# Optimization experiments

Measured on AMD Instinct MI355X. Metric: run time of the kernel, lower is better.

## Reference

```python
import jax, jax.numpy as jnp
import numpy as np

C_DIM = 128
HIDDEN = 128
RESO = 128
PADDING = 0.1


def _resnet_block(x, w0, b0, w1, b1, ws):
    # ResnetBlockFC: net = fc_0(relu(x)); dx = fc_1(relu(net)); out = shortcut(x) + dx
    net = jnp.maximum(x, 0.0) @ w0 + b0
    dx = jnp.maximum(net, 0.0) @ w1 + b1
    return x @ ws + dx


def _scatter_mean(c, index, num_seg):
    # c: (B, T, C) float, index: (B, T) int -> (B, num_seg, C), empty bins stay 0
    def one(cb, ib):
        s = jax.ops.segment_sum(cb, ib, num_segments=num_seg)
        cnt = jax.ops.segment_sum(jnp.ones((cb.shape[0],), cb.dtype), ib, num_segments=num_seg)
        return s / jnp.maximum(cnt, 1.0)[:, None]
    return jax.vmap(one)(c, index)


def setup_inputs() -> dict:
    key = jax.random.key(0)
    ks = jax.random.split(key, 12)
    B, T, D = 2, 65536, 3
    h = HIDDEN
    p = jax.random.uniform(ks[0], (B, T, D), jnp.float32, minval=-0.5, maxval=0.5)
    s = 0.02
    fc_pos_w = jax.random.normal(ks[1], (D, 2 * h), jnp.float32) * s
    fc_pos_b = jax.random.normal(ks[2], (2 * h,), jnp.float32) * s
    # 5 ResnetBlockFC blocks, all (2h -> h) since c_dim == hidden_dim
    w0 = jax.random.normal(ks[3], (5, 2 * h, h), jnp.float32) * s
    b0 = jax.random.normal(ks[4], (5, h), jnp.float32) * s
    w1 = jax.random.normal(ks[5], (5, h, h), jnp.float32) * s
    b1 = jax.random.normal(ks[6], (5, h), jnp.float32) * s
    ws = jax.random.normal(ks[7], (5, 2 * h, h), jnp.float32) * s  # shortcut, no bias
    return {"p": p, "fc_pos_w": fc_pos_w, "fc_pos_b": fc_pos_b,
            "w0": w0, "b0": b0, "w1": w1, "b1": b1, "ws": ws}


def reference(p, fc_pos_w, fc_pos_b, w0, b0, w1, b1, ws):
    # PointNet ResNet encoder
    net = p @ fc_pos_w + fc_pos_b  # (B, T, 2h)
    for i in range(5):
        hfeat = _resnet_block(net, w0[i], b0[i], w1[i], b1[i], ws[i])  # (B, T, h)
        if i < 4:
            pooled = jnp.max(hfeat, axis=1, keepdims=True)
            net = jnp.concatenate([hfeat, jnp.broadcast_to(pooled, hfeat.shape)], axis=-1)
    c = hfeat  # (B, T, c_dim)

    # normalize_coordinate(plane='xz'): take dims (0, 2), map to [0, 1)
    xy = p[..., jnp.array([0, 2])]
    xy = xy / (1.0 + PADDING + 1e-3) + 0.5
    xy = jnp.clip(xy, 0.0, 1.0 - 1e-6)
    # coordinate2index
    xi = (xy * RESO).astype(jnp.int32)
    index = xi[..., 0] + RESO * xi[..., 1]  # (B, T)

    fea = _scatter_mean(c, index, RESO * RESO)  # (B, R*R, c_dim)
    fea_plane = jnp.transpose(fea, (0, 2, 1)).reshape(p.shape[0], C_DIM, RESO, RESO)
    return fea_plane
```

## Files before the change

### kernel.cpp

```cpp
#include <hip/hip_runtime.h>
#include <hip/hip_bf16.h>


#define G_ALL 131072
#define HD    128
#define NBINS 16384

typedef __attribute__((ext_vector_type(8))) short short8;
typedef __attribute__((ext_vector_type(4))) float f32x4;

#define MFMA16(a, b, c) __builtin_amdgcn_mfma_f32_16x16x32_bf16(a, b, c, 0, 0, 0)

__device__ __forceinline__ float bf16_to_f32(unsigned short u) {
  union { unsigned int u; float f; } v; v.u = ((unsigned int)u) << 16; return v.f;
}
__device__ __forceinline__ unsigned short f32_to_bf16(float f) {
  union { float f; unsigned int u; } v; v.f = f;
  unsigned int u = v.u;
  u += 0x7fffu + ((u >> 16) & 1u);
  return (unsigned short)(u >> 16);
}
__device__ __forceinline__ unsigned int f32_key(float f) {
  union { float f; unsigned int u; } v; v.f = f;
  return (v.u & 0x80000000u) ? ~v.u : (v.u | 0x80000000u);
}
__device__ __forceinline__ float key_f32(unsigned int k) {
  union { unsigned int u; float f; } v;
  v.u = (k & 0x80000000u) ? (k & 0x7fffffffu) : ~k;
  return v.f;
}
__device__ __forceinline__ int bin_of(float p0, float p2) {
  float x = p0 / 1.101f + 0.5f;
  x = fminf(fmaxf(x, 0.0f), 1.0f - 1e-6f);
  int xi = (int)(x * 128.0f);
  float z = p2 / 1.101f + 0.5f;
  z = fminf(fmaxf(z, 0.0f), 1.0f - 1e-6f);
  int zi = (int)(z * 128.0f);
  return xi + 128 * zi;
}
__device__ __forceinline__ short8 relu8(short8 a) {
  short8 r;
#pragma unroll
  for (int e = 0; e < 8; e++) r[e] = a[e] < 0 ? (short)0 : a[e];
  return r;
}

__global__ __launch_bounds__(128) void prep_kernel(
    const float* __restrict__ fcw, const float* __restrict__ fcb,
    const float* __restrict__ ws0, float* __restrict__ Sp,
    float* __restrict__ bsp, unsigned int* __restrict__ pool,
    int* __restrict__ hist) {
  int t = blockIdx.x * 128 + threadIdx.x;
  hist[t * 2] = 0;
  hist[t * 2 + 1] = 0;
  if (t < 1024) pool[t] = 0u;
  if (blockIdx.x == 0) {
    int j = threadIdx.x;
    for (int d = 0; d < 3; d++) {
      float s = 0.f;
      for (int ch = 0; ch < 256; ch++)
        s = fmaf(fcw[d * 256 + ch], ws0[ch * HD + j], s);
      Sp[d * HD + j] = s;
    }
    float s = 0.f;
    for (int ch = 0; ch < 256; ch++)
      s = fmaf(fcb[ch], ws0[ch * HD + j], s);
    bsp[j] = s;
  }
}

__global__ __launch_bounds__(256) void wi_kernel(
    const float* __restrict__ w0, const float* __restrict__ w1,
    const float* __restrict__ ws, const float* __restrict__ p,
    unsigned short* __restrict__ B0t, unsigned short* __restrict__ W0t,
    unsigned short* __restrict__ W1t, unsigned short* __restrict__ WSt,
    int* __restrict__ hist) {
  int gid = blockIdx.x * 256 + threadIdx.x;
  if (gid >= 245760) {
    int g = gid - 245760;
    int b = g >> 16;
    int idx = bin_of(p[3 * (size_t)g], p[3 * (size_t)g + 2]);
    atomicAdd(&hist[b * NBINS + idx], 1);
    return;
  }
  float v;
  unsigned short* dstp;
  int dst;
  if (gid < 32768) {
    int n = gid >> 8, k = gid & 255;
    v = w0[k * 128 + n];
    dstp = B0t; dst = gid;
  } else if (gid < 98304) {
    int i = gid - 32768; int s = i >> 14; int n = (i >> 7) & 127; int k = i & 127;
    v = w0[(size_t)((s + 1) * 256 + k) * 128 + n];
    dstp = W0t; dst = i;
  } else if (gid < 180224) {
    int i = gid - 98304; int s = i >> 14; int n = (i >> 7) & 127; int k = i & 127;
    v = w1[(size_t)(s * 128 + k) * 128 + n];
    dstp = W1t; dst = i;
  } else {
    int i = gid - 180224; int s = i >> 14; int n = (i >> 7) & 127; int k = i & 127;
    v = ws[(size_t)((s + 1) * 256 + k) * 128 + n];
    dstp = WSt; dst = i;
  }
  dstp[dst] = f32_to_bf16(v);
}

__global__ __launch_bounds__(1024) void scan_kernel(int* __restrict__ hist,
                                                    int* __restrict__ offsets) {
  __shared__ int sd[1024];
  int t = threadIdx.x;
  int vals[32];
  int s = 0;
#pragma unroll
  for (int i = 0; i < 32; i++) { vals[i] = hist[t * 32 + i]; s += vals[i]; }
  sd[t] = s;
  __syncthreads();
  for (int d = 1; d < 1024; d <<= 1) {
    int v = (t >= d) ? sd[t - d] : 0;
    __syncthreads();
    sd[t] += v;
    __syncthreads();
  }
  int run = sd[t] - s;
#pragma unroll
  for (int i = 0; i < 32; i++) {
    offsets[t * 32 + i] = run;
    hist[t * 32 + i] = run;
    run += vals[i];
  }
  if (t == 1023) offsets[32768] = run;
}

__global__ __launch_bounds__(256) void fill_kernel(const float* __restrict__ p,
                                                   int* __restrict__ cursor,
                                                   int* __restrict__ rank) {
  int g = blockIdx.x * 256 + threadIdx.x;
  int b = g >> 16;
  int idx = bin_of(p[3 * (size_t)g], p[3 * (size_t)g + 2]);
  int pos = atomicAdd(&cursor[b * NBINS + idx], 1);
  rank[g] = pos;
}

__global__ __launch_bounds__(256) void gather_kernel(
    const unsigned short* __restrict__ cS, const int* __restrict__ offsets,
    float* __restrict__ out) {
  __shared__ float acc[129 * 65];
  const int tid = threadIdx.x;
  const int wave = tid >> 6, lane = tid & 63;
  const int B0 = blockIdx.x * 64;
  const int b = B0 >> 14;

  for (int bi = 0; bi < 16; bi++) {
    const int binL = wave * 16 + bi;
    const int B = B0 + binL;
    const int st = offsets[B], en = offsets[B + 1];
    float a0 = 0.f, a1 = 0.f;
    int k = st;
    for (; k + 2 <= en; k += 2) {
      unsigned int u0 = *(const unsigned int*)(cS + (size_t)k * HD + lane * 2);
      unsigned int u1 = *(const unsigned int*)(cS + (size_t)(k + 1) * HD + lane * 2);
      a0 += bf16_to_f32((unsigned short)(u0 & 0xffffu));
      a1 += bf16_to_f32((unsigned short)(u0 >> 16));
      a0 += bf16_to_f32((unsigned short)(u1 & 0xffffu));
      a1 += bf16_to_f32((unsigned short)(u1 >> 16));
    }
    if (k < en) {
      unsigned int u = *(const unsigned int*)(cS + (size_t)k * HD + lane * 2);
      a0 += bf16_to_f32((unsigned short)(u & 0xffffu));
      a1 += bf16_to_f32((unsigned short)(u >> 16));
    }
    acc[(2 * lane) * 65 + binL] = a0;
    acc[(2 * lane + 1) * 65 + binL] = a1;
    if (lane == 0) acc[128 * 65 + binL] = (float)(en - st);
  }
  __syncthreads();

  const size_t outBase = (size_t)b * HD * NBINS + (size_t)(B0 & (NBINS - 1));
  const float cnt = fmaxf(acc[128 * 65 + lane], 1.0f);
#pragma unroll
  for (int c2 = 0; c2 < 32; c2++) {
    int ch = wave * 32 + c2;
    out[outBase + (size_t)ch * NBINS + lane] = acc[ch * 65 + lane] / cnt;
  }
}

__global__ __launch_bounds__(512, 4) void stage0_kernel(
    const float* __restrict__ p, const float* __restrict__ fcw,
    const float* __restrict__ fcb,
    const unsigned short* __restrict__ B0t,
    const unsigned short* __restrict__ W1t,
    const float* __restrict__ b0, const float* __restrict__ b1,
    const float* __restrict__ Sp, const float* __restrict__ bsp,
    unsigned short* __restrict__ hout, unsigned int* __restrict__ pool) {
  __shared__ float fcL[1024];
  __shared__ float ptL[64 * 5];
  __shared__ unsigned short x0t[64 * 264];
  __shared__ unsigned short m2[64 * 136];
  const int tid = threadIdx.x;
  const int lane = tid & 63;
  const int q = lane >> 4, l15 = lane & 15;
  const int nt = tid >> 6;
  const int b = blockIdx.x >> 8;
  const int wrow = nt * 16 + l15;

  short8 b0w[8], w1w[4];
#pragma unroll
  for (int kc = 0; kc < 8; kc++)
    b0w[kc] = *(const short8*)(B0t + (size_t)wrow * 256 + kc * 32 + q * 8);
#pragma unroll
  for (int kc = 0; kc < 4; kc++)
    w1w[kc] = *(const short8*)(W1t + (size_t)wrow * 128 + kc * 32 + q * 8);
  const float bias1 = b0[wrow];
  const float bias2 = bsp[wrow] + b1[wrow];
  const float sp0 = Sp[wrow], sp1 = Sp[128 + wrow], sp2 = Sp[256 + wrow];

  for (int k = tid; k < 1024; k += 512)
    fcL[k] = (k < 768) ? fcw[k] : fcb[k - 768];

  for (int it = 0; it < 4; it++) {
    const int rowBase = (blockIdx.x * 4 + it) * 64;
    __syncthreads();
    if (tid < 192) ptL[(tid / 3) * 5 + (tid % 3)] = p[(size_t)rowBase * 3 + tid];
    {
      int row = tid >> 3, c8 = tid & 7;
      const float* pr = p + (size_t)(rowBase + row) * 3;
      float p0 = pr[0], p1 = pr[1], p2 = pr[2];
#pragma unroll
      for (int cc = 0; cc < 32; cc++) {
        int ch = c8 + cc * 8;
        float x = fcL[768 + ch] + p0 * fcL[ch] + p1 * fcL[256 + ch] + p2 * fcL[512 + ch];
        x0t[row * 264 + ch] = f32_to_bf16(fmaxf(x, 0.f));
      }
    }
    __syncthreads();
    f32x4 C1[4];
#pragma unroll
    for (int s = 0; s < 4; s++) C1[s] = (f32x4){bias1, bias1, bias1, bias1};
#pragma unroll
    for (int kc = 0; kc < 8; kc++) {
#pragma unroll
      for (int s = 0; s < 4; s++) {
        short8 Ar = *(const short8*)(&x0t[(s * 16 + l15) * 264 + kc * 32 + q * 8]);
        C1[s] = MFMA16(Ar, b0w[kc], C1[s]);
      }
    }
#pragma unroll
    for (int s = 0; s < 4; s++)
#pragma unroll
      for (int r = 0; r < 4; r++)
        m2[(s * 16 + q * 4 + r) * 136 + nt * 16 + l15] =
            f32_to_bf16(fmaxf(C1[s][r], 0.f));
    __syncthreads();
    f32x4 C2[4];
#pragma unroll
    for (int s = 0; s < 4; s++)
#pragma unroll
      for (int r = 0; r < 4; r++) {
        int row = s * 16 + q * 4 + r;
        C2[s][r] = bias2 + ptL[row * 5] * sp0 + ptL[row * 5 + 1] * sp1 +
                   ptL[row * 5 + 2] * sp2;
      }
#pragma unroll
    for (int kc = 0; kc < 4; kc++) {
#pragma unroll
      for (int s = 0; s < 4; s++) {
        short8 Am = *(const short8*)(&m2[(s * 16 + l15) * 136 + kc * 32 + q * 8]);
        C2[s] = MFMA16(Am, w1w[kc], C2[s]);
      }
    }
#pragma unroll
    for (int s = 0; s < 4; s++)
#pragma unroll
      for (int r = 0; r < 4; r++)
        x0t[(s * 16 + q * 4 + r) * 136 + nt * 16 + l15] = f32_to_bf16(C2[s][r]);
    {
      float m = -1e30f;
#pragma unroll
      for (int s = 0; s < 4; s++)
#pragma unroll
        for (int r = 0; r < 4; r++) m = fmaxf(m, C2[s][r]);
      m = fmaxf(m, __shfl_xor(m, 16, 64));
      m = fmaxf(m, __shfl_xor(m, 32, 64));
      if (lane < 16) atomicMax(&pool[b * 128 + nt * 16 + lane], f32_key(m));
    }
    __syncthreads();
    {
      int r = tid >> 3, cs = (tid & 7) * 16;
      short8 v0 = *(const short8*)(&x0t[r * 136 + cs]);
      short8 v1 = *(const short8*)(&x0t[r * 136 + cs + 8]);
      *(short8*)(hout + (size_t)(rowBase + r) * 128 + cs) = v0;
      *(short8*)(hout + (size_t)(rowBase + r) * 128 + cs + 8) = v1;
    }
  }
}

__global__ __launch_bounds__(512, 4) void stageN_kernel(
    const unsigned short* __restrict__ hin, unsigned short* __restrict__ hout,
    const unsigned short* __restrict__ W0t,
    const unsigned short* __restrict__ W1t,
    const unsigned short* __restrict__ WSt,
    const float* __restrict__ b0e, const float* __restrict__ bse,
    unsigned int* __restrict__ pool, int doPool,
    const int* __restrict__ rank, int useRank) {
  __shared__ unsigned short At[64 * 136];
  __shared__ unsigned short m2[64 * 136];
  const int tid = threadIdx.x;
  const int lane = tid & 63;
  const int q = lane >> 4, l15 = lane & 15;
  const int nt = tid >> 6;
  const int b = blockIdx.x >> 8;
  const int wrow = nt * 16 + l15;

  short8 w0w[4], w1w[4], wsw[4];
#pragma unroll
  for (int kc = 0; kc < 4; kc++) {
    w0w[kc] = *(const short8*)(W0t + (size_t)wrow * 128 + kc * 32 + q * 8);
    w1w[kc] = *(const short8*)(W1t + (size_t)wrow * 128 + kc * 32 + q * 8);
    wsw[kc] = *(const short8*)(WSt + (size_t)wrow * 128 + kc * 32 + q * 8);
  }
  const float bias1 = b0e[b * 128 + wrow];
  const float bias2 = bse[b * 128 + wrow];
  const int r8 = tid >> 3, cs8 = (tid & 7) * 16;

  for (int it = 0; it < 4; it++) {
    const int rowBase = (blockIdx.x * 4 + it) * 64;
    __syncthreads();
    {
      const size_t gb = ((size_t)rowBase + r8) * 128 + cs8;
      short8 v0 = *(const short8*)(hin + gb);
      short8 v1 = *(const short8*)(hin + gb + 8);
      *(short8*)(&At[r8 * 136 + cs8]) = v0;
      *(short8*)(&At[r8 * 136 + cs8 + 8]) = v1;
    }
    __syncthreads();
    f32x4 C1[4], C2[4];
#pragma unroll
    for (int s = 0; s < 4; s++) {
      C1[s] = (f32x4){bias1, bias1, bias1, bias1};
      C2[s] = (f32x4){bias2, bias2, bias2, bias2};
    }
#pragma unroll
    for (int kc = 0; kc < 4; kc++) {
#pragma unroll
      for (int s = 0; s < 4; s++) {
        short8 Ah = *(const short8*)(&At[(s * 16 + l15) * 136 + kc * 32 + q * 8]);
        short8 Ar = relu8(Ah);
        C1[s] = MFMA16(Ar, w0w[kc], C1[s]);
        C2[s] = MFMA16(Ah, wsw[kc], C2[s]);
      }
    }
#pragma unroll
    for (int s = 0; s < 4; s++)
#pragma unroll
      for (int r = 0; r < 4; r++)
        m2[(s * 16 + q * 4 + r) * 136 + nt * 16 + l15] =
            f32_to_bf16(fmaxf(C1[s][r], 0.f));
    __syncthreads();
#pragma unroll
    for (int kc = 0; kc < 4; kc++) {
#pragma unroll
      for (int s = 0; s < 4; s++) {
        short8 Am = *(const short8*)(&m2[(s * 16 + l15) * 136 + kc * 32 + q * 8]);
        C2[s] = MFMA16(Am, w1w[kc], C2[s]);
      }
    }
    if (doPool) {
      float m = -1e30f;
#pragma unroll
      for (int s = 0; s < 4; s++)
#pragma unroll
        for (int r = 0; r < 4; r++) m = fmaxf(m, C2[s][r]);
      m = fmaxf(m, __shfl_xor(m, 16, 64));
      m = fmaxf(m, __shfl_xor(m, 32, 64));
      if (lane < 16) atomicMax(&pool[b * 128 + nt * 16 + lane], f32_key(m));
    }
#pragma unroll
    for (int s = 0; s < 4; s++)
#pragma unroll
      for (int r = 0; r < 4; r++)
        At[(s * 16 + q * 4 + r) * 136 + nt * 16 + l15] = f32_to_bf16(C2[s][r]);
    __syncthreads();
    {
      int destRow = rowBase + r8;
      if (useRank) destRow = rank[destRow];
      short8 v0 = *(const short8*)(&At[r8 * 136 + cs8]);
      short8 v1 = *(const short8*)(&At[r8 * 136 + cs8 + 8]);
      *(short8*)(hout + (size_t)destRow * 128 + cs8) = v0;
      *(short8*)(hout + (size_t)destRow * 128 + cs8 + 8) = v1;
    }
  }
}

__global__ void fold_kernel(const unsigned int* __restrict__ pool,
                            const float* __restrict__ b0s,
                            const float* __restrict__ b1s,
                            const float* __restrict__ w0hi,
                            const float* __restrict__ wshi,
                            float* __restrict__ b0e, float* __restrict__ bse) {
  __shared__ float ps[256];
  int tid = threadIdx.x;
  int b = tid >> 7, j = tid & 127;
  ps[tid] = key_f32(pool[tid]);
  __syncthreads();
  float a0 = b0s[j], a1 = b1s[j];
  for (int ch = 0; ch < 128; ch++) {
    float pv = ps[b * 128 + ch];
    a0 = fmaf(fmaxf(pv, 0.f), w0hi[ch * HD + j], a0);
    a1 = fmaf(pv, wshi[ch * HD + j], a1);
  }
  b0e[b * 128 + j] = a0;
  bse[b * 128 + j] = a1;
}

extern "C" void kernel_launch(void* const* d_in, const int* in_sizes, int n_in,
                              void* d_out, int out_size, void* d_ws,
                              size_t ws_size, hipStream_t stream) {
  const float* p   = (const float*)d_in[0];
  const float* fcw = (const float*)d_in[1];
  const float* fcb = (const float*)d_in[2];
  const float* w0  = (const float*)d_in[3];
  const float* b0  = (const float*)d_in[4];
  const float* w1  = (const float*)d_in[5];
  const float* b1  = (const float*)d_in[6];
  const float* wsc = (const float*)d_in[7];
  float* out = (float*)d_out;

  char* wsp = (char*)d_ws;
  unsigned short* hA = (unsigned short*)wsp;
  unsigned short* hB = hA + (size_t)G_ALL * HD;
  unsigned short* B0t = hB + (size_t)G_ALL * HD;
  unsigned short* W0t = B0t + 32768;
  unsigned short* W1t = W0t + 65536;
  unsigned short* WSt = W1t + 81920;
  unsigned int* pool = (unsigned int*)(WSt + 65536);
  float* b0e = (float*)(pool + 1024);
  float* bse = b0e + 1024;
  float* Sp  = bse + 1024;
  float* bsp = Sp + 384;
  int* hist    = (int*)(bsp + 128);
  int* offsets = hist + 2 * NBINS;
  int* rank    = offsets + 2 * NBINS + 4;

  prep_kernel<<<128, 128, 0, stream>>>(fcw, fcb, wsc, Sp, bsp, pool, hist);
  wi_kernel<<<1472, 256, 0, stream>>>(w0, w1, wsc, p, B0t, W0t, W1t, WSt, hist);
  scan_kernel<<<1, 1024, 0, stream>>>(hist, offsets);
  fill_kernel<<<512, 256, 0, stream>>>(p, hist, rank);

  stage0_kernel<<<512, 512, 0, stream>>>(p, fcw, fcb, B0t, W1t,
                                         b0, b1, Sp, bsp, hA, pool);
  unsigned short* hin = hA;
  unsigned short* hout = hB;
  for (int s = 1; s < 5; s++) {
    fold_kernel<<<1, 256, 0, stream>>>(
        pool + (s - 1) * 256, b0 + s * HD, b1 + s * HD,
        w0 + (size_t)(s * 256 + 128) * HD, wsc + (size_t)(s * 256 + 128) * HD,
        b0e + (s - 1) * 256, bse + (s - 1) * 256);
    stageN_kernel<<<512, 512, 0, stream>>>(
        hin, hout, W0t + (s - 1) * 16384, W1t + s * 16384,
        WSt + (s - 1) * 16384, b0e + (s - 1) * 256, bse + (s - 1) * 256,
        pool + s * 256, (s < 4) ? 1 : 0, rank, (s == 4) ? 1 : 0);
    unsigned short* t = hin; hin = hout; hout = t;
  }
  gather_kernel<<<512, 256, 0, stream>>>(hin, offsets, out);
}
```

Measured before the change: 357.6 us.

## Prefetch next tile's inputs into registers and re-pad LDS rows to 140

Both MLP stage kernels now load the next 64-row tile's inputs (points in stage0, bf16 activations in stageN) into registers while the current tile is being computed, hiding global-load latency behind the MFMA work. The LDS row stride changes from 136 to 140 shorts, altering the bank mapping of the MFMA operand reads and the transposed writes. The stage0 fc_pos expansion is also restructured to write four channels at a time with vector LDS stores. The cost is more live registers under a 512x4 launch bound, and the 140 stride breaks 16-byte alignment of short8 LDS accesses on odd rows.

New measurement: 360.0 us. No clear change (+0.7%).

```diff
diff --git a/kernel.cpp b/kernel.cpp
--- a/kernel.cpp
+++ b/kernel.cpp
@@ -7,6 +7,7 @@
 #define NBINS 16384
 
 typedef __attribute__((ext_vector_type(8))) short short8;
+typedef __attribute__((ext_vector_type(4))) short short4v;
 typedef __attribute__((ext_vector_type(4))) float f32x4;
 
 #define MFMA16(a, b, c) __builtin_amdgcn_mfma_f32_16x16x32_bf16(a, b, c, 0, 0, 0)
@@ -196,13 +197,14 @@
   __shared__ float fcL[1024];
   __shared__ float ptL[64 * 5];
   __shared__ unsigned short x0t[64 * 264];
-  __shared__ unsigned short m2[64 * 136];
+  __shared__ unsigned short m2[64 * 140];
   const int tid = threadIdx.x;
   const int lane = tid & 63;
   const int q = lane >> 4, l15 = lane & 15;
   const int nt = tid >> 6;
   const int b = blockIdx.x >> 8;
   const int wrow = nt * 16 + l15;
+  const int row8 = tid >> 3, c4 = (tid & 7) * 4;
 
   short8 b0w[8], w1w[4];
 #pragma unroll
@@ -218,20 +220,36 @@
   for (int k = tid; k < 1024; k += 512)
     fcL[k] = (k < 768) ? fcw[k] : fcb[k - 768];
 
+  float pn0, pn1, pn2, pl = 0.f;
+  {
+    const int rb = blockIdx.x * 256;
+    const float* pr = p + (size_t)(rb + row8) * 3;
+    pn0 = pr[0]; pn1 = pr[1]; pn2 = pr[2];
+    if (tid < 192) pl = p[(size_t)rb * 3 + tid];
+  }
+
   for (int it = 0; it < 4; it++) {
-    const int rowBase = (blockIdx.x * 4 + it) * 64;
-    __syncthreads();
-    if (tid < 192) ptL[(tid / 3) * 5 + (tid % 3)] = p[(size_t)rowBase * 3 + tid];
-    {
-      int row = tid >> 3, c8 = tid & 7;
-      const float* pr = p + (size_t)(rowBase + row) * 3;
-      float p0 = pr[0], p1 = pr[1], p2 = pr[2];
-#pragma unroll
-      for (int cc = 0; cc < 32; cc++) {
-        int ch = c8 + cc * 8;
-        float x = fcL[768 + ch] + p0 * fcL[ch] + p1 * fcL[256 + ch] + p2 * fcL[512 + ch];
-        x0t[row * 264 + ch] = f32_to_bf16(fmaxf(x, 0.f));
-      }
+    const int rowBase = blockIdx.x * 256 + it * 64;
+    __syncthreads();
+    if (tid < 192) ptL[(tid / 3) * 5 + (tid % 3)] = pl;
+#pragma unroll
+    for (int cc = 0; cc < 8; cc++) {
+      int chb = c4 + cc * 32;
+      short4v v;
+#pragma unroll
+      for (int j = 0; j < 4; j++) {
+        int ch = chb + j;
+        float x = fcL[768 + ch] + pn0 * fcL[ch] + pn1 * fcL[256 + ch] +
+                  pn2 * fcL[512 + ch];
+        v[j] = (short)f32_to_bf16(fmaxf(x, 0.f));
+      }
+      *(short4v*)(&x0t[row8 * 264 + chb]) = v;
+    }
+    if (it < 3) {
+      const int rb = rowBase + 64;
+      const float* pr = p + (size_t)(rb + row8) * 3;
+      pn0 = pr[0]; pn1 = pr[1]; pn2 = pr[2];
+      if (tid < 192) pl = p[(size_t)rb * 3 + tid];
     }
     __syncthreads();
     f32x4 C1[4];
@@ -249,7 +267,7 @@
     for (int s = 0; s < 4; s++)
 #pragma unroll
       for (int r = 0; r < 4; r++)
-        m2[(s * 16 + q * 4 + r) * 136 + nt * 16 + l15] =
+        m2[(s * 16 + q * 4 + r) * 140 + nt * 16 + l15] =
             f32_to_bf16(fmaxf(C1[s][r], 0.f));
     __syncthreads();
     f32x4 C2[4];
@@ -265,7 +283,7 @@
     for (int kc = 0; kc < 4; kc++) {
 #pragma unroll
       for (int s = 0; s < 4; s++) {
-        short8 Am = *(const short8*)(&m2[(s * 16 + l15) * 136 + kc * 32 + q * 8]);
+        short8 Am = *(const short8*)(&m2[(s * 16 + l15) * 140 + kc * 32 + q * 8]);
         C2[s] = MFMA16(Am, w1w[kc], C2[s]);
       }
     }
@@ -273,7 +291,7 @@
     for (int s = 0; s < 4; s++)
 #pragma unroll
       for (int r = 0; r < 4; r++)
-        x0t[(s * 16 + q * 4 + r) * 136 + nt * 16 + l15] = f32_to_bf16(C2[s][r]);
+        x0t[(s * 16 + q * 4 + r) * 140 + nt * 16 + l15] = f32_to_bf16(C2[s][r]);
     {
       float m = -1e30f;
 #pragma unroll
@@ -286,11 +304,11 @@
     }
     __syncthreads();
     {
-      int r = tid >> 3, cs = (tid & 7) * 16;
-      short8 v0 = *(const short8*)(&x0t[r * 136 + cs]);
-      short8 v1 = *(const short8*)(&x0t[r * 136 + cs + 8]);
-      *(short8*)(hout + (size_t)(rowBase + r) * 128 + cs) = v0;
-      *(short8*)(hout + (size_t)(rowBase + r) * 128 + cs + 8) = v1;
+      int cs = (tid & 7) * 16;
+      short8 v0 = *(const short8*)(&x0t[row8 * 140 + cs]);
+      short8 v1 = *(const short8*)(&x0t[row8 * 140 + cs + 8]);
+      *(short8*)(hout + (size_t)(rowBase + row8) * 128 + cs) = v0;
+      *(short8*)(hout + (size_t)(rowBase + row8) * 128 + cs + 8) = v1;
     }
   }
 }
@@ -303,8 +321,8 @@
     const float* __restrict__ b0e, const float* __restrict__ bse,
     unsigned int* __restrict__ pool, int doPool,
     const int* __restrict__ rank, int useRank) {
-  __shared__ unsigned short At[64 * 136];
-  __shared__ unsigned short m2[64 * 136];
+  __shared__ unsigned short At[64 * 140];
+  __shared__ unsigned short m2[64 * 140];
   const int tid = threadIdx.x;
   const int lane = tid & 63;
   const int q = lane >> 4, l15 = lane & 15;
@@ -323,15 +341,22 @@
   const float bias2 = bse[b * 128 + wrow];
   const int r8 = tid >> 3, cs8 = (tid & 7) * 16;
 
+  short8 n0, n1;
+  {
+    const size_t gb = ((size_t)blockIdx.x * 256 + r8) * 128 + cs8;
+    n0 = *(const short8*)(hin + gb);
+    n1 = *(const short8*)(hin + gb + 8);
+  }
+
   for (int it = 0; it < 4; it++) {
-    const int rowBase = (blockIdx.x * 4 + it) * 64;
-    __syncthreads();
-    {
-      const size_t gb = ((size_t)rowBase + r8) * 128 + cs8;
-      short8 v0 = *(const short8*)(hin + gb);
-      short8 v1 = *(const short8*)(hin + gb + 8);
-      *(short8*)(&At[r8 * 136 + cs8]) = v0;
-      *(short8*)(&At[r8 * 136 + cs8 + 8]) = v1;
+    const int rowBase = blockIdx.x * 256 + it * 64;
+    __syncthreads();
+    *(short8*)(&At[r8 * 140 + cs8]) = n0;
+    *(short8*)(&At[r8 * 140 + cs8 + 8]) = n1;
+    if (it < 3) {
+      const size_t gb = ((size_t)(rowBase + 64) + r8) * 128 + cs8;
+      n0 = *(const short8*)(hin + gb);
+      n1 = *(const short8*)(hin + gb + 8);
     }
     __syncthreads();
     f32x4 C1[4], C2[4];
@@ -344,7 +369,7 @@
     for (int kc = 0; kc < 4; kc++) {
 #pragma unroll
       for (int s = 0; s < 4; s++) {
-        short8 Ah = *(const short8*)(&At[(s * 16 + l15) * 136 + kc * 32 + q * 8]);
+        short8 Ah = *(const short8*)(&At[(s * 16 + l15) * 140 + kc * 32 + q * 8]);
         short8 Ar = relu8(Ah);
         C1[s] = MFMA16(Ar, w0w[kc], C1[s]);
         C2[s] = MFMA16(Ah, wsw[kc], C2[s]);
@@ -354,14 +379,14 @@
     for (int s = 0; s < 4; s++)
 #pragma unroll
       for (int r = 0; r < 4; r++)
-        m2[(s * 16 + q * 4 + r) * 136 + nt * 16 + l15] =
+        m2[(s * 16 + q * 4 + r) * 140 + nt * 16 + l15] =
             f32_to_bf16(fmaxf(C1[s][r], 0.f));
     __syncthreads();
 #pragma unroll
     for (int kc = 0; kc < 4; kc++) {
 #pragma unroll
       for (int s = 0; s < 4; s++) {
-        short8 Am = *(const short8*)(&m2[(s * 16 + l15) * 136 + kc * 32 + q * 8]);
+        short8 Am = *(const short8*)(&m2[(s * 16 + l15) * 140 + kc * 32 + q * 8]);
         C2[s] = MFMA16(Am, w1w[kc], C2[s]);
       }
     }
@@ -379,13 +404,13 @@
     for (int s = 0; s < 4; s++)
 #pragma unroll
       for (int r = 0; r < 4; r++)
-        At[(s * 16 + q * 4 + r) * 136 + nt * 16 + l15] = f32_to_bf16(C2[s][r]);
+        At[(s * 16 + q * 4 + r) * 140 + nt * 16 + l15] = f32_to_bf16(C2[s][r]);
     __syncthreads();
     {
       int destRow = rowBase + r8;
       if (useRank) destRow = rank[destRow];
-      short8 v0 = *(const short8*)(&At[r8 * 136 + cs8]);
-      short8 v1 = *(const short8*)(&At[r8 * 136 + cs8 + 8]);
+      short8 v0 = *(const short8*)(&At[r8 * 140 + cs8]);
+      short8 v1 = *(const short8*)(&At[r8 * 140 + cs8 + 8]);
       *(short8*)(hout + (size_t)destRow * 128 + cs8) = v0;
       *(short8*)(hout + (size_t)destRow * 128 + cs8 + 8) = v1;
     }
```
